# Kernel optimization log

Measured on AMD Instinct MI355X. Metric: run time of the kernel, lower is better.

## Reference

```python
import jax, jax.numpy as jnp
import numpy as np

N, E, F, H, L, K = 50000, 1200000, 64, 64, 2, 3


def setup_inputs() -> dict:
    key = jax.random.key(0)
    ks = jax.random.split(key, 12)
    return {
        "x": jax.random.normal(ks[0], (N, F), jnp.float32),
        "edge_index": jax.random.randint(ks[1], (2, E), 0, N, dtype=jnp.int32),
        "edge_weight": jax.random.uniform(ks[2], (E,), jnp.float32),
        "h": 0.1 * jax.random.normal(ks[3], (L, N, H), jnp.float32),
        "c": 0.1 * jax.random.normal(ks[4], (L, N, H), jnp.float32),
        "Wx": 0.05 * jax.random.normal(ks[5], (L, 4, H, H), jnp.float32),
        "Wcheb": 0.05 * jax.random.normal(ks[6], (L, 4, K, H, H), jnp.float32),
        "b_cheb": 0.05 * jax.random.normal(ks[7], (L, 4, H), jnp.float32),
        "w_peep": 0.05 * jax.random.normal(ks[8], (L, 3, H), jnp.float32),
        "b_gate": 0.05 * jax.random.normal(ks[9], (L, 4, H), jnp.float32),
        "fc_w": 0.05 * jax.random.normal(ks[10], (1, H), jnp.float32),
        "fc_b": jnp.zeros((1,), jnp.float32),
    }


def _cheb_basis(hl, row, col, nw, k_order):
    # Chebyshev basis T_k(L_hat) @ h. With sym normalization and lambda_max=2
    # (PyG ChebConv default), L_hat = -D^{-1/2} A D^{-1/2} with zero diagonal.
    def prop(y):  # y: (N,H) -> L_hat @ y via edge gather + scatter-add
        return jax.ops.segment_sum(nw[:, None] * y[col], row, num_segments=N)
    tx = [hl, prop(hl)]
    for _ in range(2, k_order):
        tx.append(2.0 * prop(tx[-1]) - tx[-2])
    return jnp.stack(tx, 0)  # (K, N, H)


def reference(x, edge_index, edge_weight, h, c, Wx, Wcheb, b_cheb, w_peep, b_gate, fc_w, fc_b):
    row, col = edge_index[0], edge_index[1]
    # symmetric Laplacian normalization of edge weights
    deg = jax.ops.segment_sum(edge_weight, row, num_segments=N)
    dinv = jnp.where(deg > 0, jax.lax.rsqrt(jnp.where(deg > 0, deg, 1.0)), 0.0)
    nw = -dinv[row] * edge_weight * dinv[col]  # (E,)

    inp = x
    h_new, c_new = [], []
    for l in range(L):
        hl, cl = h[l], c[l]
        tx = _cheb_basis(hl, row, col, nw, K)  # (K,N,H), shared by all 4 gate ChebConvs
        conv = jnp.einsum('knh,gkho->gno', tx, Wcheb[l]) + b_cheb[l][:, None, :]  # (4,N,H)
        gx = jnp.einsum('nf,gfo->gno', inp, Wx[l])  # (4,N,H), gate order i,f,c,o
        i = jax.nn.sigmoid(gx[0] + conv[0] + w_peep[l, 0] * cl + b_gate[l, 0])
        f = jax.nn.sigmoid(gx[1] + conv[1] + w_peep[l, 1] * cl + b_gate[l, 1])
        t = jnp.tanh(gx[2] + conv[2] + b_gate[l, 2])
        c_t = f * cl + i * t
        o = jax.nn.sigmoid(gx[3] + conv[3] + w_peep[l, 2] * c_t + b_gate[l, 3])
        h_t = o * jnp.tanh(c_t)
        h_new.append(h_t)
        c_new.append(c_t)
        inp = h_t
    out = inp @ fc_w.T + fc_b  # (N,1); dropout p=0.0 is identity
    return out, jnp.stack(h_new), jnp.stack(c_new)
```

## Files before the change

### kernel.cpp

```cpp
#include <hip/hip_runtime.h>
#include <math.h>

#define N_NODES 50000
#define E_EDGES 1200000
#define H_DIM 64
#define L_LAYERS 2
#define CSLOT 64
#define FP8_SC 16.0f
#define FP8_ISC 0.0625f

#define SC_CHUNKS 586
#define NB_SC (8 * SC_CHUNKS)
#define NB_H  3125
#define NB_PK 512
#define ROWS_PER_RANGE 6250u

typedef __attribute__((ext_vector_type(8))) short bf16x8;
typedef __attribute__((ext_vector_type(4))) float f32x4;
typedef __attribute__((ext_vector_type(4))) unsigned int u32x4;
typedef __attribute__((ext_vector_type(4))) unsigned short u16x4;

static __device__ __forceinline__ unsigned short f2bf(float f) {
    unsigned u = __float_as_uint(f);
    unsigned r = (u + 0x7FFFu + ((u >> 16) & 1u)) >> 16;
    return (unsigned short)r;
}
static __device__ __forceinline__ float bf2f(unsigned short u) {
    return __uint_as_float(((unsigned)u) << 16);
}
static __device__ __forceinline__ unsigned short pk8(float a, float b) {
    int v = __builtin_amdgcn_cvt_pk_fp8_f32(a, b, 0, false);
    return (unsigned short)(v & 0xFFFF);
}
static __device__ __forceinline__ float f8lo(unsigned u) {
    return __builtin_amdgcn_cvt_f32_fp8((int)u, 0);
}
static __device__ __forceinline__ float f8hi(unsigned u) {
    return __builtin_amdgcn_cvt_f32_fp8((int)u, 1);
}


__global__ void prep_kernel(const int* __restrict__ row, const int* __restrict__ col,
                            const float* __restrict__ ew,
                            int* __restrict__ cnt, unsigned* __restrict__ slots4,
                            const float* __restrict__ h,
                            unsigned short* __restrict__ hbL0, unsigned short* __restrict__ hbL1,
                            const float* __restrict__ Wx, const float* __restrict__ Wcheb,
                            unsigned short* __restrict__ Wtb) {
    int b = blockIdx.x;
    int tid = threadIdx.x;
    const long NH = (long)N_NODES * H_DIM;
    if (b < NB_SC) {
        int g = b & 7;
        int eb = (b >> 3) * 2048 + tid;
        int rr[8];
#pragma unroll
        for (int t = 0; t < 8; ++t) {
            int e = eb + t * 256;
            rr[t] = (e < E_EDGES) ? __builtin_nontemporal_load(row + e) : -1;
        }
#pragma unroll
        for (int t = 0; t < 8; ++t) {
            int r = rr[t];
            if (r >= 0 && (int)((unsigned)r / ROWS_PER_RANGE) == g) {
                int e = eb + t * 256;
                int ce = __builtin_nontemporal_load(col + e);
                float we = __builtin_nontemporal_load(ew + e);
                int p = atomicAdd(&cnt[r], 1);
                if (p < CSLOT)
                    slots4[(long)r * CSLOT + p] = (unsigned)ce | ((unsigned)f2bf(we) << 16);
            }
        }
    } else if (b < NB_SC + NB_H) {
        int i = (b - NB_SC) * 256 + tid;
        f32x4 a = __builtin_nontemporal_load((const f32x4*)h + i);
        f32x4 c = __builtin_nontemporal_load((const f32x4*)(h + NH) + i);
        u16x4 o0, o1;
        o0.x = f2bf(a.x); o0.y = f2bf(a.y); o0.z = f2bf(a.z); o0.w = f2bf(a.w);
        o1.x = f2bf(c.x); o1.y = f2bf(c.y); o1.z = f2bf(c.z); o1.w = f2bf(c.w);
        __builtin_nontemporal_store(o0, (u16x4*)hbL0 + i);
        __builtin_nontemporal_store(o1, (u16x4*)hbL1 + i);
    } else {
        int i = (b - NB_SC - NB_H) * 256 + tid;
        int kk = i & 31;
        int out = (i >> 5) & 255;
        int ks = (i >> 13) & 7;
        int l = i >> 16;
        int k = ks * 32 + kk;
        int g = out >> 6;
        int o = out & 63;
        float v;
        if (k < 64) {
            v = Wx[(((l * 4 + g) * 64 + k) * 64) + o];
        } else {
            int kc = (k - 64) >> 6, hh = (k - 64) & 63;
            v = Wcheb[((((l * 4 + g) * 3 + kc) * 64 + hh) * 64) + o];
        }
        __builtin_nontemporal_store(f2bf(v), Wtb + i);
    }
}


__global__ __launch_bounds__(256) void rowsum_scale_kernel(
    const int* __restrict__ cnt, const unsigned* __restrict__ slots4,
    const unsigned short* __restrict__ hbL0, const unsigned short* __restrict__ hbL1,
    float* __restrict__ dinv, unsigned short* __restrict__ hb8s) {
    int lane = threadIdx.x & 63;
    int wv = threadIdx.x >> 6;
    int r = blockIdx.x * 4 + wv;
    if (r >= N_NODES) return;
    int ct = cnt[r]; if (ct > CSLOT) ct = CSLOT;
    unsigned s = slots4[(long)r * CSLOT + lane];
    float w = (lane < ct) ? bf2f((unsigned short)(s >> 16)) : 0.f;
#pragma unroll
    for (int off = 32; off >= 1; off >>= 1) w += __shfl_xor(w, off, 64);
    float dv = w > 0.f ? rsqrtf(w) : 0.f;
    if (lane == 0) dinv[r] = dv;
    long o = (long)r * 64 + lane;
    float f0 = bf2f(hbL0[o]) * dv * FP8_SC;
    float f1 = bf2f(hbL1[o]) * dv * FP8_SC;
    hb8s[o] = pk8(f0, f1);
}


__global__ __launch_bounds__(256) void spmv_f8_kernel(
    const int* __restrict__ cnt, const unsigned* __restrict__ slots4,
    const float* __restrict__ dinv,
    const unsigned short* __restrict__ y8,
    const unsigned short* __restrict__ baseL0, const unsigned short* __restrict__ baseL1,
    unsigned short* __restrict__ outL0, unsigned short* __restrict__ outL1,
    unsigned short* __restrict__ outS, int pass2) {
    __shared__ int s_col[4][64];
    __shared__ float s_w[4][64];
    int lane = threadIdx.x & 63;
    int wv = threadIdx.x >> 6;
    int r = blockIdx.x * 4 + wv;
    if (r >= N_NODES) return;
    int ct = cnt[r]; if (ct > CSLOT) ct = CSLOT;

    unsigned s = slots4[(long)r * CSLOT + lane];
    int cc = (int)(s & 0xFFFFu); if (cc >= N_NODES) cc = 0;
    s_col[wv][lane] = cc;
    s_w[wv][lane] = (lane < ct) ? bf2f((unsigned short)(s >> 16)) : 0.f;

    int ct8 = (ct + 7) & ~7;
    float a0 = 0.f, a1 = 0.f;
    for (int j = 0; j < ct8; j += 8) {
        unsigned u[8]; float w[8];
#pragma unroll
        for (int t = 0; t < 8; ++t) {
            int c = s_col[wv][j + t];
            w[t] = s_w[wv][j + t];
            u[t] = y8[(long)c * 64 + lane];
        }
#pragma unroll
        for (int t = 0; t < 8; ++t) {
            a0 += w[t] * f8lo(u[t]);
            a1 += w[t] * f8hi(u[t]);
        }
    }

    long o = (long)r * 64 + lane;
    float dr = dinv[r];
    if (!pass2) {
        float t0 = -dr * FP8_ISC * a0;
        float t1 = -dr * FP8_ISC * a1;
        outL0[o] = f2bf(t0);
        outL1[o] = f2bf(t1);
        outS[o] = pk8(FP8_SC * dr * t0, FP8_SC * dr * t1);
    } else {
        float t0 = -2.f * dr * FP8_ISC * a0 - bf2f(baseL0[o]);
        float t1 = -2.f * dr * FP8_ISC * a1 - bf2f(baseL1[o]);
        outL0[o] = f2bf(t0);
        outL1[o] = f2bf(t1);
    }
}


static __device__ __forceinline__ bf16x8 ldA(const unsigned short* const srcs[4],
                                             const float* __restrict__ xf, int use_f32,
                                             long rowoff, int k0) {
    if (use_f32 && k0 < 64) {
        const float* p = xf + rowoff + k0;
        f32x4 lo = *(const f32x4*)p;
        f32x4 hi = *(const f32x4*)(p + 4);
        bf16x8 r;
        r[0] = (short)f2bf(lo.x); r[1] = (short)f2bf(lo.y);
        r[2] = (short)f2bf(lo.z); r[3] = (short)f2bf(lo.w);
        r[4] = (short)f2bf(hi.x); r[5] = (short)f2bf(hi.y);
        r[6] = (short)f2bf(hi.z); r[7] = (short)f2bf(hi.w);
        return r;
    }
    return *(const bf16x8*)&srcs[k0 >> 6][rowoff + (k0 & 63)];
}

__global__ __launch_bounds__(256) void gates_mfma_kernel(
    const float* __restrict__ inp_f,
    const unsigned short* __restrict__ s_inp,
    int use_f32,
    const unsigned short* __restrict__ s_h,
    const unsigned short* __restrict__ s_t1,
    const unsigned short* __restrict__ s_t2,
    const unsigned short* __restrict__ Wtb_l,
    const float* __restrict__ b_cheb_l, const float* __restrict__ b_gate_l,
    const float* __restrict__ w_peep_l, const float* __restrict__ cl,
    float* __restrict__ h_out, float* __restrict__ c_out,
    unsigned short* __restrict__ hob, int write_hob,
    const float* __restrict__ fcw, const float* __restrict__ fcb,
    float* __restrict__ fc_out, int do_fc) {
    __shared__ __align__(16) unsigned short s_B[256][40];

    int tid = threadIdx.x;
    int nb = blockIdx.x * 64;
    int lane = tid & 63;
    int wv = tid >> 6;
    int quad = lane >> 4;
    int l16 = lane & 15;

    const unsigned short* srcs[4] = {s_inp, s_h, s_t1, s_t2};

    int nA = nb + wv * 16 + l16;
    if (nA > N_NODES - 1) nA = N_NODES - 1;
    long rowoff = (long)nA * 64;

    bf16x8 w0, w1, w2, w3, a_cur, a_nxt;
    {
        const unsigned short* bs = Wtb_l + (long)tid * 32;
        w0 = *(const bf16x8*)&bs[0];  w1 = *(const bf16x8*)&bs[8];
        w2 = *(const bf16x8*)&bs[16]; w3 = *(const bf16x8*)&bs[24];
        a_cur = ldA(srcs, inp_f, use_f32, rowoff, quad * 8);
    }

    f32x4 acc[16];
#pragma unroll
    for (int nt = 0; nt < 16; ++nt) acc[nt] = (f32x4)(0.f);

#pragma unroll
    for (int ks = 0; ks < 8; ++ks) {
        *(bf16x8*)&s_B[tid][0]  = w0;
        *(bf16x8*)&s_B[tid][8]  = w1;
        *(bf16x8*)&s_B[tid][16] = w2;
        *(bf16x8*)&s_B[tid][24] = w3;
        __syncthreads();
        if (ks < 7) {
            const unsigned short* bs = Wtb_l + ((long)(ks + 1) * 256 + tid) * 32;
            w0 = *(const bf16x8*)&bs[0];  w1 = *(const bf16x8*)&bs[8];
            w2 = *(const bf16x8*)&bs[16]; w3 = *(const bf16x8*)&bs[24];
            a_nxt = ldA(srcs, inp_f, use_f32, rowoff, (ks + 1) * 32 + quad * 8);
        }
#pragma unroll
        for (int nt = 0; nt < 16; ++nt) {
            bf16x8 b = *(const bf16x8*)&s_B[nt * 16 + l16][quad * 8];
            acc[nt] = __builtin_amdgcn_mfma_f32_16x16x32_bf16(a_cur, b, acc[nt], 0, 0, 0);
        }
        __syncthreads();
        a_cur = a_nxt;
    }

    float bias_i[4], bias_f[4], bias_t[4], bias_o[4], wp0[4], wp1[4], wp2[4], fw[4];
#pragma unroll
    for (int oc = 0; oc < 4; ++oc) {
        int o = oc * 16 + l16;
        bias_i[oc] = b_cheb_l[0 * 64 + o] + b_gate_l[0 * 64 + o];
        bias_f[oc] = b_cheb_l[1 * 64 + o] + b_gate_l[1 * 64 + o];
        bias_t[oc] = b_cheb_l[2 * 64 + o] + b_gate_l[2 * 64 + o];
        bias_o[oc] = b_cheb_l[3 * 64 + o] + b_gate_l[3 * 64 + o];
        wp0[oc] = w_peep_l[0 * 64 + o];
        wp1[oc] = w_peep_l[1 * 64 + o];
        wp2[oc] = w_peep_l[2 * 64 + o];
        fw[oc] = do_fc ? fcw[o] : 0.f;
    }
    float fcb0 = do_fc ? fcb[0] : 0.f;

#pragma unroll
    for (int r = 0; r < 4; ++r) {
        int n = nb + wv * 16 + quad * 4 + r;
        if (n < N_NODES) {
            float fcs = 0.f;
#pragma unroll
            for (int oc = 0; oc < 4; ++oc) {
                int o = oc * 16 + l16;
                long off = (long)n * 64 + o;
                float cv = cl[off];
                float gi = acc[0 * 4 + oc][r] + bias_i[oc] + wp0[oc] * cv;
                float gf = acc[1 * 4 + oc][r] + bias_f[oc] + wp1[oc] * cv;
                float gt = acc[2 * 4 + oc][r] + bias_t[oc];
                float go = acc[3 * 4 + oc][r] + bias_o[oc];
                float ig = 1.f / (1.f + __expf(-gi));
                float fg = 1.f / (1.f + __expf(-gf));
                float tg = tanhf(gt);
                float ct = fg * cv + ig * tg;
                float og = 1.f / (1.f + __expf(-(go + wp2[oc] * ct)));
                float ht = og * tanhf(ct);
                h_out[off] = ht;
                c_out[off] = ct;
                if (write_hob) hob[off] = f2bf(ht);
                fcs += ht * fw[oc];
            }
            if (do_fc) {
                fcs += __shfl_xor(fcs, 1, 64);
                fcs += __shfl_xor(fcs, 2, 64);
                fcs += __shfl_xor(fcs, 4, 64);
                fcs += __shfl_xor(fcs, 8, 64);
                if (l16 == 0) fc_out[n] = fcs + fcb0;
            }
        }
    }
}

extern "C" void kernel_launch(void* const* d_in, const int* in_sizes, int n_in,
                              void* d_out, int out_size, void* d_ws, size_t ws_size,
                              hipStream_t stream) {
    const float* x      = (const float*)d_in[0];
    const int*   ei     = (const int*)d_in[1];
    const float* ew     = (const float*)d_in[2];
    const float* h      = (const float*)d_in[3];
    const float* c      = (const float*)d_in[4];
    const float* Wx     = (const float*)d_in[5];
    const float* Wcheb  = (const float*)d_in[6];
    const float* b_cheb = (const float*)d_in[7];
    const float* w_peep = (const float*)d_in[8];
    const float* b_gate = (const float*)d_in[9];
    const float* fc_w   = (const float*)d_in[10];
    const float* fc_b   = (const float*)d_in[11];
    float* out = (float*)d_out;

    const int* row = ei;
    const int* col = ei + E_EDGES;
    const long NH = (long)N_NODES * H_DIM;

    float* W = (float*)d_ws;
    int*      cnt    = (int*)W;
    float*    dinv   = W + 50000;
    unsigned* slots4 = (unsigned*)(W + 100000);
    unsigned short* hbL0  = (unsigned short*)(slots4 + (long)N_NODES * CSLOT);
    unsigned short* hbL1  = hbL0 + NH;
    unsigned short* tx1L0 = hbL1 + NH;
    unsigned short* tx1L1 = tx1L0 + NH;
    unsigned short* tx2L0 = tx1L1 + NH;
    unsigned short* tx2L1 = tx2L0 + NH;
    unsigned short* hb8s  = tx2L1 + NH;
    unsigned short* t18s  = hb8s + NH;
    unsigned short* hob   = t18s + NH;
    unsigned short* Wtb   = hob + NH;

    hipMemsetAsync(cnt, 0, N_NODES * sizeof(int), stream);
    prep_kernel<<<NB_SC + NB_H + NB_PK, 256, 0, stream>>>(
        row, col, ew, cnt, slots4, h, hbL0, hbL1, Wx, Wcheb, Wtb);
    rowsum_scale_kernel<<<(N_NODES + 3) / 4, 256, 0, stream>>>(cnt, slots4, hbL0, hbL1, dinv, hb8s);

    spmv_f8_kernel<<<(N_NODES + 3) / 4, 256, 0, stream>>>(
        cnt, slots4, dinv, hb8s, (const unsigned short*)nullptr, (const unsigned short*)nullptr,
        tx1L0, tx1L1, t18s, 0);
    spmv_f8_kernel<<<(N_NODES + 3) / 4, 256, 0, stream>>>(
        cnt, slots4, dinv, t18s, hbL0, hbL1,
        tx2L0, tx2L1, (unsigned short*)nullptr, 1);

    float* h_out_base = out + N_NODES;
    float* c_out_base = out + N_NODES + (long)L_LAYERS * NH;

    gates_mfma_kernel<<<(N_NODES + 63) / 64, 256, 0, stream>>>(
        x, hob, 1, hbL0, tx1L0, tx2L0, Wtb,
        b_cheb, b_gate, w_peep, c,
        h_out_base, c_out_base, hob, 1,
        fc_w, fc_b, out, 0);
    gates_mfma_kernel<<<(N_NODES + 63) / 64, 256, 0, stream>>>(
        x, hob, 0, hbL1, tx1L1, tx2L1, Wtb + (long)8 * 256 * 32,
        b_cheb + 4 * 64, b_gate + 4 * 64, w_peep + 3 * 64, c + NH,
        h_out_base + NH, c_out_base + NH, hob, 0,
        fc_w, fc_b, out, 1);
}
```

Measured before the change: 336.5 us.

## Stage full gate weight matrix in LDS once and compute 32 rows per wave

The packed weight layout changes to row-major [out][k], and the gates kernel now loads the whole 256x256 bf16 weight matrix into shared memory once per block. Previously it streamed 32-wide K slices with two barriers per step. Blocks grow to 512 threads covering 256 nodes, and each wave computes two 16-row tiles that share every B fragment. This amortizes weight loading and removes per-step synchronization, at the cost of about 132KB of LDS per block and doubled accumulator registers, which may limit occupancy.

```diff
diff --git a/kernel.cpp b/kernel.cpp
--- a/kernel.cpp
+++ b/kernel.cpp
@@ -82,11 +82,9 @@
         __builtin_nontemporal_store(o1, (u16x4*)hbL1 + i);
     } else {
         int i = (b - NB_SC - NB_H) * 256 + tid;
-        int kk = i & 31;
-        int out = (i >> 5) & 255;
-        int ks = (i >> 13) & 7;
+        int k = i & 255;
+        int out = (i >> 8) & 255;
         int l = i >> 16;
-        int k = ks * 32 + kk;
         int g = out >> 6;
         int o = out & 63;
         float v;
@@ -194,7 +192,7 @@
     return *(const bf16x8*)&srcs[k0 >> 6][rowoff + (k0 & 63)];
 }
 
-__global__ __launch_bounds__(256) void gates_mfma_kernel(
+__global__ __launch_bounds__(512, 2) void gates_mfma_kernel(
     const float* __restrict__ inp_f,
     const unsigned short* __restrict__ s_inp,
     int use_f32,
@@ -208,53 +206,62 @@
     unsigned short* __restrict__ hob, int write_hob,
     const float* __restrict__ fcw, const float* __restrict__ fcb,
     float* __restrict__ fc_out, int do_fc) {
-    __shared__ __align__(16) unsigned short s_B[256][40];
+    __shared__ __align__(16) unsigned short s_B[256][264];
 
     int tid = threadIdx.x;
-    int nb = blockIdx.x * 64;
+    int nb = blockIdx.x * 256;
     int lane = tid & 63;
     int wv = tid >> 6;
     int quad = lane >> 4;
     int l16 = lane & 15;
 
+    {
+        bf16x8 wr[8];
+#pragma unroll
+        for (int half = 0; half < 2; ++half) {
+#pragma unroll
+            for (int j = 0; j < 8; ++j) {
+                int idx = tid + (half * 8 + j) * 512;
+                wr[j] = *(const bf16x8*)&Wtb_l[(long)idx * 8];
+            }
+#pragma unroll
+            for (int j = 0; j < 8; ++j) {
+                int idx = tid + (half * 8 + j) * 512;
+                *(bf16x8*)&s_B[idx >> 5][(idx & 31) * 8] = wr[j];
+            }
+        }
+    }
+
     const unsigned short* srcs[4] = {s_inp, s_h, s_t1, s_t2};
 
-    int nA = nb + wv * 16 + l16;
-    if (nA > N_NODES - 1) nA = N_NODES - 1;
-    long rowoff = (long)nA * 64;
-
-    bf16x8 w0, w1, w2, w3, a_cur, a_nxt;
-    {
-        const unsigned short* bs = Wtb_l + (long)tid * 32;
-        w0 = *(const bf16x8*)&bs[0];  w1 = *(const bf16x8*)&bs[8];
-        w2 = *(const bf16x8*)&bs[16]; w3 = *(const bf16x8*)&bs[24];
-        a_cur = ldA(srcs, inp_f, use_f32, rowoff, quad * 8);
-    }
-
-    f32x4 acc[16];
-#pragma unroll
-    for (int nt = 0; nt < 16; ++nt) acc[nt] = (f32x4)(0.f);
+    int nA0 = nb + wv * 32 + l16;      if (nA0 > N_NODES - 1) nA0 = N_NODES - 1;
+    int nA1 = nb + wv * 32 + 16 + l16; if (nA1 > N_NODES - 1) nA1 = N_NODES - 1;
+    long ro0 = (long)nA0 * 64, ro1 = (long)nA1 * 64;
+
+    f32x4 acc0[16], acc1[16];
+#pragma unroll
+    for (int nt = 0; nt < 16; ++nt) { acc0[nt] = (f32x4)(0.f); acc1[nt] = (f32x4)(0.f); }
+
+    bf16x8 a0c = ldA(srcs, inp_f, use_f32, ro0, quad * 8);
+    bf16x8 a1c = ldA(srcs, inp_f, use_f32, ro1, quad * 8);
+
+    __syncthreads();
 
 #pragma unroll
     for (int ks = 0; ks < 8; ++ks) {
-        *(bf16x8*)&s_B[tid][0]  = w0;
-        *(bf16x8*)&s_B[tid][8]  = w1;
-        *(bf16x8*)&s_B[tid][16] = w2;
-        *(bf16x8*)&s_B[tid][24] = w3;
-        __syncthreads();
+        bf16x8 a0n = a0c, a1n = a1c;
         if (ks < 7) {
-            const unsigned short* bs = Wtb_l + ((long)(ks + 1) * 256 + tid) * 32;
-            w0 = *(const bf16x8*)&bs[0];  w1 = *(const bf16x8*)&bs[8];
-            w2 = *(const bf16x8*)&bs[16]; w3 = *(const bf16x8*)&bs[24];
-            a_nxt = ldA(srcs, inp_f, use_f32, rowoff, (ks + 1) * 32 + quad * 8);
+            int k0n = (ks + 1) * 32 + quad * 8;
+            a0n = ldA(srcs, inp_f, use_f32, ro0, k0n);
+            a1n = ldA(srcs, inp_f, use_f32, ro1, k0n);
         }
 #pragma unroll
         for (int nt = 0; nt < 16; ++nt) {
-            bf16x8 b = *(const bf16x8*)&s_B[nt * 16 + l16][quad * 8];
-            acc[nt] = __builtin_amdgcn_mfma_f32_16x16x32_bf16(a_cur, b, acc[nt], 0, 0, 0);
-        }
-        __syncthreads();
-        a_cur = a_nxt;
+            bf16x8 b = *(const bf16x8*)&s_B[nt * 16 + l16][ks * 32 + quad * 8];
+            acc0[nt] = __builtin_amdgcn_mfma_f32_16x16x32_bf16(a0c, b, acc0[nt], 0, 0, 0);
+            acc1[nt] = __builtin_amdgcn_mfma_f32_16x16x32_bf16(a1c, b, acc1[nt], 0, 0, 0);
+        }
+        a0c = a0n; a1c = a1n;
     }
 
     float bias_i[4], bias_f[4], bias_t[4], bias_o[4], wp0[4], wp1[4], wp2[4], fw[4];
@@ -272,40 +279,45 @@
     }
     float fcb0 = do_fc ? fcb[0] : 0.f;
 
-#pragma unroll
-    for (int r = 0; r < 4; ++r) {
-        int n = nb + wv * 16 + quad * 4 + r;
-        if (n < N_NODES) {
-            float fcs = 0.f;
-#pragma unroll
-            for (int oc = 0; oc < 4; ++oc) {
-                int o = oc * 16 + l16;
-                long off = (long)n * 64 + o;
-                float cv = cl[off];
-                float gi = acc[0 * 4 + oc][r] + bias_i[oc] + wp0[oc] * cv;
-                float gf = acc[1 * 4 + oc][r] + bias_f[oc] + wp1[oc] * cv;
-                float gt = acc[2 * 4 + oc][r] + bias_t[oc];
-                float go = acc[3 * 4 + oc][r] + bias_o[oc];
-                float ig = 1.f / (1.f + __expf(-gi));
-                float fg = 1.f / (1.f + __expf(-gf));
-                float tg = tanhf(gt);
-                float ct = fg * cv + ig * tg;
-                float og = 1.f / (1.f + __expf(-(go + wp2[oc] * ct)));
-                float ht = og * tanhf(ct);
-                h_out[off] = ht;
-                c_out[off] = ct;
-                if (write_hob) hob[off] = f2bf(ht);
-                fcs += ht * fw[oc];
-            }
-            if (do_fc) {
-                fcs += __shfl_xor(fcs, 1, 64);
-                fcs += __shfl_xor(fcs, 2, 64);
-                fcs += __shfl_xor(fcs, 4, 64);
-                fcs += __shfl_xor(fcs, 8, 64);
-                if (l16 == 0) fc_out[n] = fcs + fcb0;
-            }
-        }
-    }
+#define GATE_EPILOG(ACC, MOFF)                                                        \
+    _Pragma("unroll")                                                                 \
+    for (int r = 0; r < 4; ++r) {                                                     \
+        int n = nb + wv * 32 + (MOFF) + quad * 4 + r;                                 \
+        if (n < N_NODES) {                                                            \
+            float fcs = 0.f;                                                          \
+            _Pragma("unroll")                                                         \
+            for (int oc = 0; oc < 4; ++oc) {                                          \
+                int o = oc * 16 + l16;                                                \
+                long off = (long)n * 64 + o;                                          \
+                float cv = cl[off];                                                   \
+                float gi = ACC[0 * 4 + oc][r] + bias_i[oc] + wp0[oc] * cv;            \
+                float gf = ACC[1 * 4 + oc][r] + bias_f[oc] + wp1[oc] * cv;            \
+                float gt = ACC[2 * 4 + oc][r] + bias_t[oc];                           \
+                float go = ACC[3 * 4 + oc][r] + bias_o[oc];                           \
+                float ig = 1.f / (1.f + __expf(-gi));                                 \
+                float fg = 1.f / (1.f + __expf(-gf));                                 \
+                float tg = tanhf(gt);                                                 \
+                float ct = fg * cv + ig * tg;                                         \
+                float og = 1.f / (1.f + __expf(-(go + wp2[oc] * ct)));                \
+                float ht = og * tanhf(ct);                                            \
+                h_out[off] = ht;                                                      \
+                c_out[off] = ct;                                                      \
+                if (write_hob) hob[off] = f2bf(ht);                                   \
+                fcs += ht * fw[oc];                                                   \
+            }                                                                         \
+            if (do_fc) {                                                              \
+                fcs += __shfl_xor(fcs, 1, 64);                                        \
+                fcs += __shfl_xor(fcs, 2, 64);                                        \
+                fcs += __shfl_xor(fcs, 4, 64);                                        \
+                fcs += __shfl_xor(fcs, 8, 64);                                        \
+                if (l16 == 0) fc_out[n] = fcs + fcb0;                                 \
+            }                                                                         \
+        }                                                                             \
+    }
+
+    GATE_EPILOG(acc0, 0)
+    GATE_EPILOG(acc1, 16)
+#undef GATE_EPILOG
 }
 
 extern "C" void kernel_launch(void* const* d_in, const int* in_sizes, int n_in,
@@ -359,13 +371,15 @@
     float* h_out_base = out + N_NODES;
     float* c_out_base = out + N_NODES + (long)L_LAYERS * NH;
 
-    gates_mfma_kernel<<<(N_NODES + 63) / 64, 256, 0, stream>>>(
+    int gates_grid = (N_NODES + 255) / 256;
+
+    gates_mfma_kernel<<<gates_grid, 512, 0, stream>>>(
         x, hob, 1, hbL0, tx1L0, tx2L0, Wtb,
         b_cheb, b_gate, w_peep, c,
         h_out_base, c_out_base, hob, 1,
         fc_w, fc_b, out, 0);
-    gates_mfma_kernel<<<(N_NODES + 63) / 64, 256, 0, stream>>>(
-        x, hob, 0, hbL1, tx1L1, tx2L1, Wtb + (long)8 * 256 * 32,
+    gates_mfma_kernel<<<gates_grid, 512, 0, stream>>>(
+        x, hob, 0, hbL1, tx1L1, tx2L1, Wtb + (long)256 * 256,
         b_cheb + 4 * 64, b_gate + 4 * 64, w_peep + 3 * 64, c + NH,
         h_out_base + NH, c_out_base + NH, hob, 0,
         fc_w, fc_b, out, 1);
```

Measured after the change: 329.9 us. 2.0% less time.
